# Performance work log

Measured on AMD Instinct MI355X. Metric: run time of the kernel, lower is better.

## Reference

```python
import jax, jax.numpy as jnp
import numpy as np

EPS = 1e-6
NUM_HEADS = 16
D_K = 64
D_V = 64

def _feat(x):
    # elu(x) + 1 feature map (positive)
    return jax.nn.elu(x) + 1.0

def setup_inputs() -> dict:
    key = jax.random.key(0)
    ks = jax.random.split(key, 11)
    B, S, D = 4, 8192, 1024
    s = 1.0 / np.sqrt(D)
    return {
        "query": jax.random.normal(ks[0], (B, S, D), jnp.float32),
        "key":   jax.random.normal(ks[1], (B, S, D), jnp.float32),
        "value": jax.random.normal(ks[2], (B, S, D), jnp.float32),
        "Wq": jax.random.normal(ks[3], (D, D), jnp.float32) * s,
        "bq": jax.random.normal(ks[4], (D,), jnp.float32) * 0.01,
        "Wk": jax.random.normal(ks[5], (D, D), jnp.float32) * s,
        "bk": jax.random.normal(ks[6], (D,), jnp.float32) * 0.01,
        "Wv": jax.random.normal(ks[7], (D, D), jnp.float32) * s,
        "bv": jax.random.normal(ks[8], (D,), jnp.float32) * 0.01,
        "Wo": jax.random.normal(ks[9], (D, D), jnp.float32) * s,
        "bo": jax.random.normal(ks[10], (D,), jnp.float32) * 0.01,
    }

def reference(query, key, value, Wq, bq, Wk, bk, Wv, bv, Wo, bo):
    B, T, _ = query.shape
    H, dk, dv = NUM_HEADS, D_K, D_V
    # projections + elu+1 feature map on q, k (value is plain linear)
    q = _feat(query @ Wq.T + bq).reshape(B, T, H, dk)
    k = _feat(key   @ Wk.T + bk).reshape(B, -1, H, dk)
    v = (value @ Wv.T + bv).reshape(B, -1, H, dv)
    # O(N) linear attention chain
    kv = jnp.einsum('bshd,bshk->bhkd', k, v)            # [B,H,dv,dk]
    norm = 1.0 / (jnp.einsum('bthd,bhd->bth', q, k.sum(axis=1)) + EPS)  # [B,T,H]
    attn = jnp.einsum('bthd,bhkd,bth->bthk', q, kv, norm)               # [B,T,H,dv]
    out = attn.reshape(B, T, H * dv) @ Wo.T + bo
    return out
```

## Files before the change

kernel.cpp:

```cpp
#include <hip/hip_runtime.h>

typedef __bf16 bf16;
typedef __bf16 bf16x4 __attribute__((ext_vector_type(4)));
typedef __bf16 bf16x8 __attribute__((ext_vector_type(8)));
typedef float  f32x4  __attribute__((ext_vector_type(4)));

__device__ __forceinline__ void gld16(const bf16* g, bf16* l) {
  __builtin_amdgcn_global_load_lds((const __attribute__((address_space(1))) void*)g,
                                   (__attribute__((address_space(3))) void*)l, 16, 0, 0);
}

__global__ void wcvt(const float* __restrict__ w0, const float* __restrict__ w1,
                     const float* __restrict__ w2, const float* __restrict__ w3,
                     bf16* __restrict__ dst)
{
  const int m = blockIdx.x >> 10;
  const float* src = (m == 0) ? w0 : (m == 1) ? w1 : (m == 2) ? w2 : w3;
  const int i = ((blockIdx.x & 1023) * 256 + threadIdx.x) * 4;
  f32x4 v = *(const f32x4*)(src + i);
  bf16x4 o;
  #pragma unroll
  for (int j = 0; j < 4; ++j) o[j] = (bf16)v[j];
  *(bf16x4*)(dst + (size_t)m * (1024 * 1024) + i) = o;
}

template<int FEAT, typename OutT>
__global__ __launch_bounds__(256, 2)
void gemm_af32(const float* __restrict__ A, const bf16* __restrict__ W,
               const float* __restrict__ bias, OutT* __restrict__ out,
               int M, int N, int K)
{
  __shared__ __align__(16) bf16 at[128*32];
  __shared__ __align__(16) bf16 bt[128*32];
  const int tid  = threadIdx.x;
  const int wave = tid >> 6;
  const int lane = tid & 63;
  const int quad = lane >> 4;
  const int l15  = lane & 15;

  const int q8 = gridDim.x >> 3;
  int id = blockIdx.x;
  id = (id & 7) * q8 + (id >> 3);
  const long row0 = (long)(id >> 3) * 128;
  const long col0 = (long)(id & 7) * 128;
  const int wm = wave >> 1, wn = wave & 1;

  f32x4 acc[4][4] = {};

  const int ar = tid >> 3;
  const int ac = (tid & 7) * 4;
  const float* Ap = A + (row0 + ar) * (long)K + ac;

  const int r0 = wave*16 + (lane>>2);
  const int ca = (lane&3)*8;
  const bf16* Bp0 = W + (col0 + r0      )*(long)K + ca;
  const bf16* Bp1 = W + (col0 + r0 + 64 )*(long)K + ca;
  bf16* lB0 = bt +        wave*512;
  bf16* lB1 = bt + 2048 + wave*512;

  for (int k0 = 0; k0 < K; k0 += 32) {
    __syncthreads();
    gld16(Bp0 + k0, lB0);
    gld16(Bp1 + k0, lB1);
    #pragma unroll
    for (int j = 0; j < 4; ++j) {
      f32x4 a4 = *(const f32x4*)(Ap + (long)j * 32 * K + k0);
      bf16x4 b4;
      #pragma unroll
      for (int i = 0; i < 4; ++i) b4[i] = (bf16)a4[i];
      *(bf16x4*)(at + (j*32 + ar)*32 + ac) = b4;
    }
    __syncthreads();
    bf16x8 af[4], bv[4];
    #pragma unroll
    for (int t = 0; t < 4; ++t)
      af[t] = *(const bf16x8*)(at + (wm*64 + t*16 + l15)*32 + quad*8);
    #pragma unroll
    for (int t = 0; t < 4; ++t)
      bv[t] = *(const bf16x8*)(bt + (wn*64 + t*16 + l15)*32 + quad*8);
    #pragma unroll
    for (int i = 0; i < 4; ++i)
      #pragma unroll
      for (int j = 0; j < 4; ++j)
        acc[i][j] = __builtin_amdgcn_mfma_f32_16x16x32_bf16(af[i], bv[j], acc[i][j], 0, 0, 0);
  }

  #pragma unroll
  for (int i = 0; i < 4; ++i) {
    #pragma unroll
    for (int j = 0; j < 4; ++j) {
      const long col = col0 + wn*64 + j*16 + l15;
      const float bb = bias[col];
      #pragma unroll
      for (int r = 0; r < 4; ++r) {
        const long row = row0 + wm*64 + i*16 + quad*4 + r;
        float v = acc[i][j][r] + bb;
        if (FEAT) v = (v > 0.f) ? (v + 1.f) : __expf(v);
        out[row*(long)N + col] = (OutT)v;
      }
    }
  }
}

template<int FEAT, typename OutT>
__global__ __launch_bounds__(256, 2)
void gemm_abf16(const bf16* __restrict__ A, const bf16* __restrict__ W,
                const float* __restrict__ bias, OutT* __restrict__ out,
                int M, int N, int K)
{
  __shared__ __align__(16) bf16 at[128*32];
  __shared__ __align__(16) bf16 bt[128*32];
  const int tid  = threadIdx.x;
  const int wave = tid >> 6;
  const int lane = tid & 63;
  const int quad = lane >> 4;
  const int l15  = lane & 15;

  const int q8 = gridDim.x >> 3;
  int id = blockIdx.x;
  id = (id & 7) * q8 + (id >> 3);
  const long row0 = (long)(id >> 3) * 128;
  const long col0 = (long)(id & 7) * 128;
  const int wm = wave >> 1, wn = wave & 1;

  f32x4 acc[4][4] = {};

  const int r0 = wave*16 + (lane>>2);
  const int ca = (lane&3)*8;
  const bf16* Ap0 = A + (row0 + r0      )*(long)K + ca;
  const bf16* Ap1 = A + (row0 + r0 + 64 )*(long)K + ca;
  const bf16* Bp0 = W + (col0 + r0      )*(long)K + ca;
  const bf16* Bp1 = W + (col0 + r0 + 64 )*(long)K + ca;
  bf16* lA0 = at +        wave*512;
  bf16* lA1 = at + 2048 + wave*512;
  bf16* lB0 = bt +        wave*512;
  bf16* lB1 = bt + 2048 + wave*512;

  for (int k0 = 0; k0 < K; k0 += 32) {
    __syncthreads();
    gld16(Ap0 + k0, lA0);
    gld16(Ap1 + k0, lA1);
    gld16(Bp0 + k0, lB0);
    gld16(Bp1 + k0, lB1);
    __syncthreads();
    bf16x8 af[4], bv[4];
    #pragma unroll
    for (int t = 0; t < 4; ++t)
      af[t] = *(const bf16x8*)(at + (wm*64 + t*16 + l15)*32 + quad*8);
    #pragma unroll
    for (int t = 0; t < 4; ++t)
      bv[t] = *(const bf16x8*)(bt + (wn*64 + t*16 + l15)*32 + quad*8);
    #pragma unroll
    for (int i = 0; i < 4; ++i)
      #pragma unroll
      for (int j = 0; j < 4; ++j)
        acc[i][j] = __builtin_amdgcn_mfma_f32_16x16x32_bf16(af[i], bv[j], acc[i][j], 0, 0, 0);
  }

  #pragma unroll
  for (int i = 0; i < 4; ++i) {
    #pragma unroll
    for (int j = 0; j < 4; ++j) {
      const long col = col0 + wn*64 + j*16 + l15;
      const float bb = bias[col];
      #pragma unroll
      for (int r = 0; r < 4; ++r) {
        const long row = row0 + wm*64 + i*16 + quad*4 + r;
        float v = acc[i][j][r] + bb;
        if (FEAT) v = (v > 0.f) ? (v + 1.f) : __expf(v);
        out[row*(long)N + col] = (OutT)v;
      }
    }
  }
}

__global__ __launch_bounds__(256, 2)
void kv_kernel(const bf16* __restrict__ Kc, const bf16* __restrict__ Vc,
               float* __restrict__ kvacc, float* __restrict__ ksum, int s_off)
{
  __shared__ __align__(16) bf16 kT[64*32];
  __shared__ __align__(16) bf16 vT[64*32];
  __shared__ float ksl[64];
  const int tid = threadIdx.x, wave = tid >> 6, lane = tid & 63;
  const int quad = lane >> 4, l15 = lane & 15;
  const int h = blockIdx.x;
  const long sbase = (long)blockIdx.y * 1024;
  const int b = (int)((s_off + sbase) >> 13);
  const int bh = b * 16 + h;
  const bf16* Kp = Kc + h * 64;
  const bf16* Vp = Vc + h * 64;

  if (tid < 64) ksl[tid] = 0.f;
  f32x4 acc[4] = {};
  float ks[8] = {};
  const int sld = tid >> 3;
  const int d0  = (tid & 7) * 8;

  for (int it = 0; it < 32; ++it) {
    const long s0 = sbase + it * 32;
    __syncthreads();
    bf16x8 k8 = *(const bf16x8*)(Kp + (s0 + sld) * 1024 + d0);
    bf16x8 v8 = *(const bf16x8*)(Vp + (s0 + sld) * 1024 + d0);
    #pragma unroll
    for (int i = 0; i < 8; ++i) {
      kT[(d0 + i) * 32 + sld] = k8[i];
      vT[(d0 + i) * 32 + sld] = v8[i];
      ks[i] += (float)k8[i];
    }
    __syncthreads();
    bf16x8 af = *(const bf16x8*)(vT + (wave*16 + l15)*32 + quad*8);
    #pragma unroll
    for (int tj = 0; tj < 4; ++tj) {
      bf16x8 bv = *(const bf16x8*)(kT + (tj*16 + l15)*32 + quad*8);
      acc[tj] = __builtin_amdgcn_mfma_f32_16x16x32_bf16(af, bv, acc[tj], 0, 0, 0);
    }
  }

  float* outp = kvacc + (long)bh * 4096;
  #pragma unroll
  for (int tj = 0; tj < 4; ++tj)
    #pragma unroll
    for (int r = 0; r < 4; ++r) {
      int m = wave*16 + quad*4 + r;
      int n = tj*16 + l15;
      atomicAdd(outp + m*64 + n, acc[tj][r]);
    }

  #pragma unroll
  for (int i = 0; i < 8; ++i) atomicAdd(&ksl[d0 + i], ks[i]);
  __syncthreads();
  if (tid < 64) atomicAdd(ksum + bh*64 + tid, ksl[tid]);
}

__global__ void kv_pack(const float* __restrict__ kvacc, bf16* __restrict__ kvb)
{
  const int i = (blockIdx.x * 256 + threadIdx.x) * 4;
  f32x4 v = *(const f32x4*)(kvacc + i);
  #pragma unroll
  for (int j = 0; j < 4; ++j) kvb[i + j] = (bf16)v[j];
}

__global__ __launch_bounds__(256, 2)
void attn_kernel(const bf16* Q, const bf16* __restrict__ kvb,
                 const float* __restrict__ ksum, bf16* attn)
{
  const int T = 8192;
  __shared__ __align__(16) bf16 qt[2*128*32];
  __shared__ __align__(16) bf16 kvt[80*72];
  __shared__ float denoml[128];
  const int tid = threadIdx.x, wave = tid >> 6, lane = tid & 63;
  const int quad = lane >> 4, l15 = lane & 15;
  const int bh = blockIdx.y;
  const long t0 = (long)blockIdx.x * 128;
  const bf16* Qp = Q + ((long)(bh >> 4) * T + t0) * 1024 + (bh & 15) * 64;

  for (int c = wave; c < 16; c += 4) {
    int kc  = c >> 3;
    int row = (c & 7) * 16 + (lane >> 2);
    int col = kc * 32 + (lane & 3) * 8;
    gld16(Qp + (long)row * 1024 + col, qt + c * 512);
  }
  const bf16* kvpb = kvb + (long)bh * 4096;
  #pragma unroll
  for (int j = 0; j < 2; ++j) {
    int e = (j*256 + tid) * 8;
    int row = e >> 6, col = e & 63;
    *(bf16x8*)(kvt + row*72 + col) = *(const bf16x8*)(kvpb + e);
  }
  if (tid < 64) kvt[64*72 + tid] = (bf16)ksum[bh*64 + tid];
  if (tid < 240) {
    int row = 65 + (tid >> 4);
    int col = (tid & 15) * 4;
    #pragma unroll
    for (int i = 0; i < 4; ++i) kvt[row*72 + col + i] = (bf16)0.f;
  }
  __syncthreads();

  f32x4 acc[2][4] = {}; f32x4 accd[2] = {};
  #pragma unroll
  for (int kc = 0; kc < 2; ++kc) {
    bf16x8 af[2], bv[5];
    #pragma unroll
    for (int i = 0; i < 2; ++i)
      af[i] = *(const bf16x8*)(qt + kc*4096 + (wave*32 + i*16 + l15)*32 + quad*8);
    #pragma unroll
    for (int j = 0; j < 5; ++j)
      bv[j] = *(const bf16x8*)(kvt + (j*16 + l15)*72 + kc*32 + quad*8);
    #pragma unroll
    for (int i = 0; i < 2; ++i) {
      #pragma unroll
      for (int j = 0; j < 4; ++j)
        acc[i][j] = __builtin_amdgcn_mfma_f32_16x16x32_bf16(af[i], bv[j], acc[i][j], 0, 0, 0);
      accd[i] = __builtin_amdgcn_mfma_f32_16x16x32_bf16(af[i], bv[4], accd[i], 0, 0, 0);
    }
  }
  if (l15 == 0) {
    #pragma unroll
    for (int i = 0; i < 2; ++i)
      #pragma unroll
      for (int r = 0; r < 4; ++r)
        denoml[wave*32 + i*16 + quad*4 + r] = accd[i][r];
  }
  __syncthreads();

  bf16* ap = attn + ((long)(bh >> 4) * T + t0) * 1024 + (bh & 15) * 64;
  #pragma unroll
  for (int i = 0; i < 2; ++i)
    #pragma unroll
    for (int r = 0; r < 4; ++r) {
      int m = wave*32 + i*16 + quad*4 + r;
      float nrm = 1.f / (denoml[m] + 1e-6f);
      #pragma unroll
      for (int j = 0; j < 4; ++j)
        ap[(long)m*1024 + j*16 + l15] = (bf16)(acc[i][j][r] * nrm);
    }
}

extern "C" void kernel_launch(void* const* d_in, const int* in_sizes, int n_in,
                              void* d_out, int out_size, void* d_ws, size_t ws_size,
                              hipStream_t stream)
{
  const int S = 8192, D = 1024, M = 4 * S;
  const float* query = (const float*)d_in[0];
  const float* key   = (const float*)d_in[1];
  const float* value = (const float*)d_in[2];
  const float* Wq = (const float*)d_in[3];  const float* bq = (const float*)d_in[4];
  const float* Wk = (const float*)d_in[5];  const float* bk = (const float*)d_in[6];
  const float* Wv = (const float*)d_in[7];  const float* bv = (const float*)d_in[8];
  const float* Wo = (const float*)d_in[9];  const float* bo = (const float*)d_in[10];

  const size_t fixed = (size_t)M * D * sizeof(bf16)
                     + (size_t)4 * D * D * sizeof(bf16)
                     + (size_t)(64 * 4096 + 4096) * sizeof(float)
                     + (size_t)64 * 4096 * sizeof(bf16);
  int CR = 4096;
  for (int cand = 32768; cand > 4096; cand >>= 1)
    if (fixed + (size_t)2 * cand * D * sizeof(bf16) <= ws_size) { CR = cand; break; }

  bf16*  QA    = (bf16*)d_ws;
  bf16*  Kc    = QA + (size_t)M * D;
  bf16*  Vc    = Kc + (size_t)CR * D;
  bf16*  Wb    = Vc + (size_t)CR * D;
  bf16*  Wqb = Wb, *Wkb = Wb + (size_t)D*D, *Wvb = Wb + (size_t)2*D*D, *Wob = Wb + (size_t)3*D*D;
  float* kvacc = (float*)(Wb + (size_t)4 * D * D);
  float* ksum  = kvacc + 64 * 4096;
  bf16*  kvb   = (bf16*)(ksum + 4096);

  dim3 blk(256);

  wcvt<<<dim3(4096), blk, 0, stream>>>(Wq, Wk, Wv, Wo, Wb);
  hipMemsetAsync(kvacc, 0, (64 * 4096 + 4096) * sizeof(float), stream);
  gemm_af32<1, bf16><<<dim3((M/128)*8), blk, 0, stream>>>(query, Wqb, bq, QA, M, D, D);
  for (int c = 0; c < M / CR; ++c) {
    const float* krows = key   + (size_t)c * CR * D;
    const float* vrows = value + (size_t)c * CR * D;
    gemm_af32<1, bf16><<<dim3((CR/128)*8), blk, 0, stream>>>(krows, Wkb, bk, Kc, CR, D, D);
    gemm_af32<0, bf16><<<dim3((CR/128)*8), blk, 0, stream>>>(vrows, Wvb, bv, Vc, CR, D, D);
    kv_kernel<<<dim3(16, CR/1024), blk, 0, stream>>>(Kc, Vc, kvacc, ksum, c * CR);
  }
  kv_pack<<<dim3(256), blk, 0, stream>>>(kvacc, kvb);
  attn_kernel<<<dim3(S/128, 64), blk, 0, stream>>>(QA, kvb, ksum, QA);
  gemm_abf16<0, float><<<dim3((M/128)*8), blk, 0, stream>>>(QA, Wob, bo, (float*)d_out, M, D, D);
}
```

Measured before the change: 846.5 us.

## Double-buffer LDS tiles in GEMM and KV kernels to overlap loads with MFMA

Adds ping-pong shared-memory buffers to both GEMM kernels and the KV reduction kernel. The next K-slice is prefetched into the alternate buffer while MFMAs run on the current one, cutting one barrier per iteration. The aim is to hide global-load latency behind compute. In exchange, LDS use doubles, which could lower occupancy, and register pressure rises from holding prefetched fp32 A values.

```diff
diff --git a/kernel.cpp b/kernel.cpp
--- a/kernel.cpp
+++ b/kernel.cpp
@@ -30,8 +30,8 @@
                const float* __restrict__ bias, OutT* __restrict__ out,
                int M, int N, int K)
 {
-  __shared__ __align__(16) bf16 at[128*32];
-  __shared__ __align__(16) bf16 bt[128*32];
+  __shared__ __align__(16) bf16 at[2][128*32];
+  __shared__ __align__(16) bf16 bt[2][128*32];
   const int tid  = threadIdx.x;
   const int wave = tid >> 6;
   const int lane = tid & 63;
@@ -55,34 +55,57 @@
   const int ca = (lane&3)*8;
   const bf16* Bp0 = W + (col0 + r0      )*(long)K + ca;
   const bf16* Bp1 = W + (col0 + r0 + 64 )*(long)K + ca;
-  bf16* lB0 = bt +        wave*512;
-  bf16* lB1 = bt + 2048 + wave*512;
+
+  gld16(Bp0, &bt[0][wave*512]);
+  gld16(Bp1, &bt[0][2048 + wave*512]);
+  {
+    f32x4 a4[4];
+    #pragma unroll
+    for (int j = 0; j < 4; ++j) a4[j] = *(const f32x4*)(Ap + (long)j * 32 * K);
+    #pragma unroll
+    for (int j = 0; j < 4; ++j) {
+      bf16x4 b4;
+      #pragma unroll
+      for (int i = 0; i < 4; ++i) b4[i] = (bf16)a4[j][i];
+      *(bf16x4*)(&at[0][(j*32 + ar)*32 + ac]) = b4;
+    }
+  }
+  __syncthreads();
 
   for (int k0 = 0; k0 < K; k0 += 32) {
-    __syncthreads();
-    gld16(Bp0 + k0, lB0);
-    gld16(Bp1 + k0, lB1);
-    #pragma unroll
-    for (int j = 0; j < 4; ++j) {
-      f32x4 a4 = *(const f32x4*)(Ap + (long)j * 32 * K + k0);
-      bf16x4 b4;
-      #pragma unroll
-      for (int i = 0; i < 4; ++i) b4[i] = (bf16)a4[i];
-      *(bf16x4*)(at + (j*32 + ar)*32 + ac) = b4;
-    }
-    __syncthreads();
+    const int cur = (k0 >> 5) & 1;
+    const int nxt = cur ^ 1;
+    const bool more = (k0 + 32 < K);
+    f32x4 a4[4];
+    if (more) {
+      gld16(Bp0 + k0 + 32, &bt[nxt][wave*512]);
+      gld16(Bp1 + k0 + 32, &bt[nxt][2048 + wave*512]);
+      #pragma unroll
+      for (int j = 0; j < 4; ++j)
+        a4[j] = *(const f32x4*)(Ap + (long)j * 32 * K + k0 + 32);
+    }
     bf16x8 af[4], bv[4];
     #pragma unroll
     for (int t = 0; t < 4; ++t)
-      af[t] = *(const bf16x8*)(at + (wm*64 + t*16 + l15)*32 + quad*8);
+      af[t] = *(const bf16x8*)(&at[cur][(wm*64 + t*16 + l15)*32 + quad*8]);
     #pragma unroll
     for (int t = 0; t < 4; ++t)
-      bv[t] = *(const bf16x8*)(bt + (wn*64 + t*16 + l15)*32 + quad*8);
+      bv[t] = *(const bf16x8*)(&bt[cur][(wn*64 + t*16 + l15)*32 + quad*8]);
     #pragma unroll
     for (int i = 0; i < 4; ++i)
       #pragma unroll
       for (int j = 0; j < 4; ++j)
         acc[i][j] = __builtin_amdgcn_mfma_f32_16x16x32_bf16(af[i], bv[j], acc[i][j], 0, 0, 0);
+    if (more) {
+      #pragma unroll
+      for (int j = 0; j < 4; ++j) {
+        bf16x4 b4;
+        #pragma unroll
+        for (int i = 0; i < 4; ++i) b4[i] = (bf16)a4[j][i];
+        *(bf16x4*)(&at[nxt][(j*32 + ar)*32 + ac]) = b4;
+      }
+    }
+    __syncthreads();
   }
 
   #pragma unroll
@@ -108,8 +131,8 @@
                 const float* __restrict__ bias, OutT* __restrict__ out,
                 int M, int N, int K)
 {
-  __shared__ __align__(16) bf16 at[128*32];
-  __shared__ __align__(16) bf16 bt[128*32];
+  __shared__ __align__(16) bf16 at[2][128*32];
+  __shared__ __align__(16) bf16 bt[2][128*32];
   const int tid  = threadIdx.x;
   const int wave = tid >> 6;
   const int lane = tid & 63;
@@ -131,30 +154,36 @@
   const bf16* Ap1 = A + (row0 + r0 + 64 )*(long)K + ca;
   const bf16* Bp0 = W + (col0 + r0      )*(long)K + ca;
   const bf16* Bp1 = W + (col0 + r0 + 64 )*(long)K + ca;
-  bf16* lA0 = at +        wave*512;
-  bf16* lA1 = at + 2048 + wave*512;
-  bf16* lB0 = bt +        wave*512;
-  bf16* lB1 = bt + 2048 + wave*512;
+
+  gld16(Ap0, &at[0][wave*512]);
+  gld16(Ap1, &at[0][2048 + wave*512]);
+  gld16(Bp0, &bt[0][wave*512]);
+  gld16(Bp1, &bt[0][2048 + wave*512]);
+  __syncthreads();
 
   for (int k0 = 0; k0 < K; k0 += 32) {
-    __syncthreads();
-    gld16(Ap0 + k0, lA0);
-    gld16(Ap1 + k0, lA1);
-    gld16(Bp0 + k0, lB0);
-    gld16(Bp1 + k0, lB1);
-    __syncthreads();
+    const int cur = (k0 >> 5) & 1;
+    const int nxt = cur ^ 1;
+    const bool more = (k0 + 32 < K);
+    if (more) {
+      gld16(Ap0 + k0 + 32, &at[nxt][wave*512]);
+      gld16(Ap1 + k0 + 32, &at[nxt][2048 + wave*512]);
+      gld16(Bp0 + k0 + 32, &bt[nxt][wave*512]);
+      gld16(Bp1 + k0 + 32, &bt[nxt][2048 + wave*512]);
+    }
     bf16x8 af[4], bv[4];
     #pragma unroll
     for (int t = 0; t < 4; ++t)
-      af[t] = *(const bf16x8*)(at + (wm*64 + t*16 + l15)*32 + quad*8);
+      af[t] = *(const bf16x8*)(&at[cur][(wm*64 + t*16 + l15)*32 + quad*8]);
     #pragma unroll
     for (int t = 0; t < 4; ++t)
-      bv[t] = *(const bf16x8*)(bt + (wn*64 + t*16 + l15)*32 + quad*8);
+      bv[t] = *(const bf16x8*)(&bt[cur][(wn*64 + t*16 + l15)*32 + quad*8]);
     #pragma unroll
     for (int i = 0; i < 4; ++i)
       #pragma unroll
       for (int j = 0; j < 4; ++j)
         acc[i][j] = __builtin_amdgcn_mfma_f32_16x16x32_bf16(af[i], bv[j], acc[i][j], 0, 0, 0);
+    __syncthreads();
   }
 
   #pragma unroll
@@ -178,8 +207,8 @@
 void kv_kernel(const bf16* __restrict__ Kc, const bf16* __restrict__ Vc,
                float* __restrict__ kvacc, float* __restrict__ ksum, int s_off)
 {
-  __shared__ __align__(16) bf16 kT[64*32];
-  __shared__ __align__(16) bf16 vT[64*32];
+  __shared__ __align__(16) bf16 kT[2][64*32];
+  __shared__ __align__(16) bf16 vT[2][64*32];
   __shared__ float ksl[64];
   const int tid = threadIdx.x, wave = tid >> 6, lane = tid & 63;
   const int quad = lane >> 4, l15 = lane & 15;
@@ -196,24 +225,42 @@
   const int sld = tid >> 3;
   const int d0  = (tid & 7) * 8;
 
+  {
+    bf16x8 k8 = *(const bf16x8*)(Kp + (sbase + sld) * 1024 + d0);
+    bf16x8 v8 = *(const bf16x8*)(Vp + (sbase + sld) * 1024 + d0);
+    #pragma unroll
+    for (int i = 0; i < 8; ++i) {
+      kT[0][(d0 + i) * 32 + sld] = k8[i];
+      vT[0][(d0 + i) * 32 + sld] = v8[i];
+      ks[i] += (float)k8[i];
+    }
+  }
+  __syncthreads();
+
   for (int it = 0; it < 32; ++it) {
-    const long s0 = sbase + it * 32;
+    const int cur = it & 1, nxt = cur ^ 1;
+    const bool more = (it + 1 < 32);
+    bf16x8 k8, v8;
+    if (more) {
+      const long s0 = sbase + (it + 1) * 32;
+      k8 = *(const bf16x8*)(Kp + (s0 + sld) * 1024 + d0);
+      v8 = *(const bf16x8*)(Vp + (s0 + sld) * 1024 + d0);
+    }
+    bf16x8 af = *(const bf16x8*)(&vT[cur][(wave*16 + l15)*32 + quad*8]);
+    #pragma unroll
+    for (int tj = 0; tj < 4; ++tj) {
+      bf16x8 bv = *(const bf16x8*)(&kT[cur][(tj*16 + l15)*32 + quad*8]);
+      acc[tj] = __builtin_amdgcn_mfma_f32_16x16x32_bf16(af, bv, acc[tj], 0, 0, 0);
+    }
+    if (more) {
+      #pragma unroll
+      for (int i = 0; i < 8; ++i) {
+        kT[nxt][(d0 + i) * 32 + sld] = k8[i];
+        vT[nxt][(d0 + i) * 32 + sld] = v8[i];
+        ks[i] += (float)k8[i];
+      }
+    }
     __syncthreads();
-    bf16x8 k8 = *(const bf16x8*)(Kp + (s0 + sld) * 1024 + d0);
-    bf16x8 v8 = *(const bf16x8*)(Vp + (s0 + sld) * 1024 + d0);
-    #pragma unroll
-    for (int i = 0; i < 8; ++i) {
-      kT[(d0 + i) * 32 + sld] = k8[i];
-      vT[(d0 + i) * 32 + sld] = v8[i];
-      ks[i] += (float)k8[i];
-    }
-    __syncthreads();
-    bf16x8 af = *(const bf16x8*)(vT + (wave*16 + l15)*32 + quad*8);
-    #pragma unroll
-    for (int tj = 0; tj < 4; ++tj) {
-      bf16x8 bv = *(const bf16x8*)(kT + (tj*16 + l15)*32 + quad*8);
-      acc[tj] = __builtin_amdgcn_mfma_f32_16x16x32_bf16(af, bv, acc[tj], 0, 0, 0);
-    }
   }
 
   float* outp = kvacc + (long)bh * 4096;
```

New measurement: 849.9 us. Within noise of the previous version (+0.4%).
